# Optimization experiments

Measured on AMD Instinct MI355X. Metric: run time of the kernel, lower is better.

## Reference

```python
import jax, jax.numpy as jnp
import numpy as np

B, S, HID = 4, 1024, 2048
H, KV, D = 16, 4, 128  # query heads, kv heads, head_dim
ROPE_THETA = 1e6


def setup_inputs() -> dict:
    key = jax.random.key(0)
    ks = jax.random.split(key, 5)
    x = jax.random.normal(ks[0], (B, S, HID), dtype=jnp.float32)
    wq = jax.random.normal(ks[1], (HID, H * D), dtype=jnp.float32) / np.sqrt(HID)
    wk = jax.random.normal(ks[2], (HID, KV * D), dtype=jnp.float32) / np.sqrt(HID)
    wv = jax.random.normal(ks[3], (HID, KV * D), dtype=jnp.float32) / np.sqrt(HID)
    wo = jax.random.normal(ks[4], (H * D, HID), dtype=jnp.float32) / np.sqrt(H * D)
    # RoPE tables: freqs duplicated to head_dim (HF convention matching rotate_half)
    inv_freq = 1.0 / (ROPE_THETA ** (jnp.arange(0, D, 2, dtype=jnp.float32) / D))
    ang = jnp.arange(S, dtype=jnp.float32)[:, None] * inv_freq[None, :]  # [S, D/2]
    emb = jnp.concatenate([ang, ang], axis=-1)  # [S, D]
    return {"x": x, "cos": jnp.cos(emb), "sin": jnp.sin(emb),
            "wq": wq, "wk": wk, "wv": wv, "wo": wo}


def _rotate_half(t):
    half = t.shape[-1] // 2
    return jnp.concatenate([-t[..., half:], t[..., :half]], axis=-1)


def reference(x, cos, sin, wq, wk, wv, wo):
    b, s, _ = x.shape
    q = (x @ wq).reshape(b, s, H, D)
    k = (x @ wk).reshape(b, s, KV, D)
    v = (x @ wv).reshape(b, s, KV, D)
    # RoPE: cos/sin [S,D] broadcast over heads (unsqueeze_dim=1 -> [S,1,D])
    c = cos[:, None, :]
    sn = sin[:, None, :]
    q = q * c + _rotate_half(q) * sn
    k = k * c + _rotate_half(k) * sn
    # repeat_kv: each kv head repeated n_repeat times consecutively
    rep = H // KV
    k = jnp.repeat(k, rep, axis=2)  # [B,S,H,D]
    v = jnp.repeat(v, rep, axis=2)
    # [B,H,S,D]
    q = q.transpose(0, 2, 1, 3)
    k = k.transpose(0, 2, 1, 3)
    v = v.transpose(0, 2, 1, 3)
    scores = jnp.einsum("bhqd,bhkd->bhqk", q, k) / jnp.sqrt(jnp.float32(D))
    causal = jnp.tril(jnp.ones((s, s), dtype=bool))
    scores = jnp.where(causal, scores, -jnp.inf)
    probs = jax.nn.softmax(scores.astype(jnp.float32), axis=-1).astype(q.dtype)
    out = jnp.einsum("bhqk,bhkd->bhqd", probs, v)
    out = out.transpose(0, 2, 1, 3).reshape(b, s, H * D)
    return out @ wo
```

## Files before the change

kernel.cpp:

```cpp
#include <hip/hip_runtime.h>

typedef __attribute__((ext_vector_type(8))) __bf16 bf16x8;
typedef __attribute__((ext_vector_type(4))) __bf16 bf16x4;
typedef __attribute__((ext_vector_type(4))) float f32x4;

#define DEV static __device__ __forceinline__

DEV void gload_lds16(const void* g, void* l) {
  __builtin_amdgcn_global_load_lds((const __attribute__((address_space(1))) void*)g,
                                   (__attribute__((address_space(3))) void*)l, 16, 0, 0);
}

DEV void lgkm0_sb() {
  asm volatile("s_waitcnt lgkmcnt(0)" ::: "memory");
  __builtin_amdgcn_sched_barrier(0);
}

__global__ void cvt_kernel(const float* __restrict__ src, __bf16* __restrict__ dst, int n) {
  int i = (blockIdx.x * 256 + threadIdx.x) * 8;
  if (i >= n) return;
  float4 a = *(const float4*)(src + i);
  float4 b = *(const float4*)(src + i + 4);
  bf16x8 o;
  o[0] = (__bf16)a.x; o[1] = (__bf16)a.y; o[2] = (__bf16)a.z; o[3] = (__bf16)a.w;
  o[4] = (__bf16)b.x; o[5] = (__bf16)b.y; o[6] = (__bf16)b.z; o[7] = (__bf16)b.w;
  *(bf16x8*)(dst + i) = o;
}

__global__ void tcvt_kernel(const float* __restrict__ src, __bf16* __restrict__ dst, int K, int N) {
  __shared__ float tile[32][33];
  int k0 = blockIdx.y * 32, n0 = blockIdx.x * 32;
  int tx = threadIdx.x & 31, ty = threadIdx.x >> 5;
  #pragma unroll
  for (int i = 0; i < 32; i += 8)
    tile[ty + i][tx] = src[(size_t)(k0 + ty + i) * N + n0 + tx];
  __syncthreads();
  #pragma unroll
  for (int i = 0; i < 32; i += 8)
    dst[(size_t)(n0 + ty + i) * K + k0 + tx] = (__bf16)tile[tx][ty + i];
}

__global__ void vt_kernel(const __bf16* __restrict__ QKV, __bf16* __restrict__ VT) {
  __shared__ __bf16 t[32][33];
  int sx = blockIdx.x;
  int dx = blockIdx.y;
  int bk = blockIdx.z;
  int b = bk >> 2, kvh = bk & 3;
  int tx = threadIdx.x & 31, ty = threadIdx.x >> 5;
  #pragma unroll
  for (int i = 0; i < 32; i += 8)
    t[ty + i][tx] = QKV[(size_t)(b * 1024 + sx * 32 + ty + i) * 3072 + 2560 + kvh * 128 + dx * 32 + tx];
  __syncthreads();
  #pragma unroll
  for (int i = 0; i < 32; i += 8)
    VT[((size_t)bk * 128 + dx * 32 + ty + i) * 1024 + sx * 32 + tx] = t[tx][ty + i];
}

template <int BM, typename OutT>
__global__ __launch_bounds__(512, 2) void gemm8p(const __bf16* __restrict__ A,
                                                 const __bf16* __restrict__ Bt,
                                                 OutT* __restrict__ C,
                                                 int M, int N, int K) {
  constexpr int ABYTES = BM * 64 * 2;
  constexpr int BBYTES = 256 * 64 * 2;
  constexpr int MH = BM / 64;
  __shared__ alignas(1024) char smem[2 * (ABYTES + BBYTES)];

  const int tid = threadIdx.x;
  const int l = tid & 63, w = tid >> 6;
  const int wr = w >> 2, wc = w & 3;
  const int g = l >> 4, ln = l & 15;

  const int nbx = gridDim.x;
  const int nwg = nbx * gridDim.y;
  int lin = blockIdx.y * nbx + blockIdx.x;
  lin = (lin & 7) * (nwg >> 3) + (lin >> 3);
  const int brow = (lin / nbx) * BM, bcol = (lin % nbx) * 256;

  const __bf16* Ag = A + (size_t)brow * K;
  const __bf16* Bg = Bt + (size_t)bcol * K;
  const int NT = K / 64;

  auto Abuf = [&](int buf) -> char* { return smem + buf * ABYTES; };
  auto Bbuf = [&](int buf) -> char* { return smem + 2 * ABYTES + buf * BBYTES; };

  f32x4 acc[2 * MH][4] = {};

  auto chunk = [&](const __bf16* gb, char* lb, int ktc, int sub) {
    int r16 = l >> 2;
    int colb = ((l & 3) * 16) ^ (((l >> 5) & 1) << 5);
    int row = (sub >> 1) * 16 + r16;
    gload_lds16(gb + (size_t)row * K + ktc * 64 + (sub & 1) * 32 + (colb >> 1),
                lb + sub * 1024 + l * 16);
  };
  auto stA0 = [&](int ktc, int buf) {
    if constexpr (BM == 256) {
      #pragma unroll
      for (int i = 0; i < 2; ++i) { int idx = i * 8 + w; chunk(Ag, Abuf(buf), ktc, (idx >> 3) * 16 + (idx & 7)); }
    } else {
      chunk(Ag, Abuf(buf), ktc, (w >> 2) * 8 + (w & 3));
    }
  };
  auto stA1 = [&](int ktc, int buf) {
    if constexpr (BM == 256) {
      #pragma unroll
      for (int i = 0; i < 2; ++i) { int idx = i * 8 + w; chunk(Ag, Abuf(buf), ktc, 8 + (idx >> 3) * 16 + (idx & 7)); }
    } else {
      chunk(Ag, Abuf(buf), ktc, 4 + (w >> 2) * 8 + (w & 3));
    }
  };
  auto stB0 = [&](int ktc, int buf) {
    #pragma unroll
    for (int i = 0; i < 2; ++i) { int idx = i * 8 + w; chunk(Bg, Bbuf(buf), ktc, (idx >> 2) * 8 + (idx & 3)); }
  };
  auto stB1 = [&](int ktc, int buf) {
    #pragma unroll
    for (int i = 0; i < 2; ++i) { int idx = i * 8 + w; chunk(Bg, Bbuf(buf), ktc, 4 + (idx >> 2) * 8 + (idx & 3)); }
  };

  auto ldA = [&](int buf, int m, int kk) -> bf16x8 {
    int sub = (wr * (BM / 32) + m) * 2 + kk;
    return *(const bf16x8*)(Abuf(buf) + sub * 1024 + ln * 64 + ((g * 16) ^ (((ln >> 3) & 1) << 5)));
  };
  auto ldB = [&](int buf, int n, int kk) -> bf16x8 {
    int sub = (wc * 4 + n) * 2 + kk;
    return *(const bf16x8*)(Bbuf(buf) + sub * 1024 + ln * 64 + ((g * 16) ^ (((ln >> 3) & 1) << 5)));
  };

  auto vmw = [&](int which) {
    if constexpr (BM == 256) {
      if (which == 0) asm volatile("s_waitcnt vmcnt(10)" ::: "memory");
      else if (which == 1) asm volatile("s_waitcnt vmcnt(12)" ::: "memory");
      else asm volatile("s_waitcnt vmcnt(12)" ::: "memory");
    } else {
      if (which == 0) asm volatile("s_waitcnt vmcnt(7)" ::: "memory");
      else if (which == 1) asm volatile("s_waitcnt vmcnt(9)" ::: "memory");
      else asm volatile("s_waitcnt vmcnt(9)" ::: "memory");
    }
    __builtin_amdgcn_sched_barrier(0);
  };
  auto bar = [&]() {
    __builtin_amdgcn_sched_barrier(0);
    __builtin_amdgcn_s_barrier();
    __builtin_amdgcn_sched_barrier(0);
  };

  stA0(0, 0); stB0(0, 0); stB1(0, 0); stA1(0, 0);
  stA0(1, 1); stB0(1, 1); stB1(1, 1); stA1(1, 1);
  vmw(2);
  bar();

  bf16x8 af[MH][2], bf[4][2];

  for (int kt = 0; kt < NT; ++kt) {
    const int buf = kt & 1;
    const int ktc = (kt + 2) & 31;

    #pragma unroll
    for (int m = 0; m < MH; ++m) { af[m][0] = ldA(buf, m, 0); af[m][1] = ldA(buf, m, 1); }
    #pragma unroll
    for (int n = 0; n < 2; ++n) { bf[n][0] = ldB(buf, n, 0); bf[n][1] = ldB(buf, n, 1); }
    bar();
    lgkm0_sb();
    __builtin_amdgcn_s_setprio(1);
    #pragma unroll
    for (int m = 0; m < MH; ++m)
      #pragma unroll
      for (int n = 0; n < 2; ++n)
        #pragma unroll
        for (int kk = 0; kk < 2; ++kk)
          acc[m][n] = __builtin_amdgcn_mfma_f32_16x16x32_bf16(af[m][kk], bf[n][kk], acc[m][n], 0, 0, 0);
    __builtin_amdgcn_s_setprio(0);
    vmw(0);
    bar();

    #pragma unroll
    for (int n = 2; n < 4; ++n) { bf[n][0] = ldB(buf, n, 0); bf[n][1] = ldB(buf, n, 1); }
    stA0(ktc, buf); stB0(ktc, buf);
    bar();
    lgkm0_sb();
    __builtin_amdgcn_s_setprio(1);
    #pragma unroll
    for (int m = 0; m < MH; ++m)
      #pragma unroll
      for (int n = 2; n < 4; ++n)
        #pragma unroll
        for (int kk = 0; kk < 2; ++kk)
          acc[m][n] = __builtin_amdgcn_mfma_f32_16x16x32_bf16(af[m][kk], bf[n][kk], acc[m][n], 0, 0, 0);
    __builtin_amdgcn_s_setprio(0);
    vmw(1);
    bar();

    #pragma unroll
    for (int m = 0; m < MH; ++m) { af[m][0] = ldA(buf, MH + m, 0); af[m][1] = ldA(buf, MH + m, 1); }
    stB1(ktc, buf);
    bar();
    lgkm0_sb();
    __builtin_amdgcn_s_setprio(1);
    #pragma unroll
    for (int m = 0; m < MH; ++m)
      #pragma unroll
      for (int n = 0; n < 2; ++n)
        #pragma unroll
        for (int kk = 0; kk < 2; ++kk)
          acc[MH + m][n] = __builtin_amdgcn_mfma_f32_16x16x32_bf16(af[m][kk], bf[n][kk], acc[MH + m][n], 0, 0, 0);
    __builtin_amdgcn_s_setprio(0);
    bar();

    stA1(ktc, buf);
    bar();
    lgkm0_sb();
    __builtin_amdgcn_s_setprio(1);
    #pragma unroll
    for (int m = 0; m < MH; ++m)
      #pragma unroll
      for (int n = 2; n < 4; ++n)
        #pragma unroll
        for (int kk = 0; kk < 2; ++kk)
          acc[MH + m][n] = __builtin_amdgcn_mfma_f32_16x16x32_bf16(af[m][kk], bf[n][kk], acc[MH + m][n], 0, 0, 0);
    __builtin_amdgcn_s_setprio(0);
    vmw(2);
    bar();
  }

  #pragma unroll
  for (int mi = 0; mi < 2 * MH; ++mi)
    #pragma unroll
    for (int n = 0; n < 4; ++n)
      #pragma unroll
      for (int j = 0; j < 4; ++j) {
        size_t r = brow + wr * (BM / 2) + mi * 16 + g * 4 + j;
        size_t c = bcol + wc * 64 + n * 16 + ln;
        C[r * N + c] = (OutT)acc[mi][n][j];
      }
}

__global__ __launch_bounds__(512, 2) void gemm8p_qkv(const __bf16* __restrict__ A,
                                                     const __bf16* __restrict__ Bt,
                                                     __bf16* __restrict__ C,
                                                     int M, int N, int K) {
  constexpr int ABYTES = 256 * 64 * 2;
  constexpr int BBYTES = 192 * 64 * 2;
  __shared__ alignas(1024) char smem[2 * (ABYTES + BBYTES)];

  const int tid = threadIdx.x;
  const int l = tid & 63, w = tid >> 6;
  const int wr = w >> 2, wc = w & 3;
  const int g = l >> 4, ln = l & 15;

  const int nbx = gridDim.x;
  const int nwg = nbx * gridDim.y;
  int lin = blockIdx.y * nbx + blockIdx.x;
  lin = (lin & 7) * (nwg >> 3) + (lin >> 3);
  const int brow = (lin / nbx) * 256, bcol = (lin % nbx) * 192;

  const __bf16* Ag = A + (size_t)brow * K;
  const __bf16* Bg = Bt + (size_t)bcol * K;
  const int NT = K / 64;

  auto Abuf = [&](int buf) -> char* { return smem + buf * ABYTES; };
  auto Bbuf = [&](int buf) -> char* { return smem + 2 * ABYTES + buf * BBYTES; };

  f32x4 acc[8][3] = {};

  auto chunk = [&](const __bf16* gb, char* lb, int ktc, int sub) {
    int r16 = l >> 2;
    int colb = ((l & 3) * 16) ^ (((l >> 5) & 1) << 5);
    int row = (sub >> 1) * 16 + r16;
    gload_lds16(gb + (size_t)row * K + ktc * 64 + (sub & 1) * 32 + (colb >> 1),
                lb + sub * 1024 + l * 16);
  };
  auto stA0 = [&](int ktc, int buf) {
    #pragma unroll
    for (int i = 0; i < 2; ++i) { int idx = i * 8 + w; chunk(Ag, Abuf(buf), ktc, (idx >> 3) * 16 + (idx & 7)); }
  };
  auto stA1 = [&](int ktc, int buf) {
    #pragma unroll
    for (int i = 0; i < 2; ++i) { int idx = i * 8 + w; chunk(Ag, Abuf(buf), ktc, 8 + (idx >> 3) * 16 + (idx & 7)); }
  };
  auto stBg0 = [&](int ktc, int buf) {
    #pragma unroll
    for (int i = 0; i < 2; ++i) {
      int t = i * 8 + w;
      int sub = ((t >> 2) * 3 + ((t >> 1) & 1)) * 2 + (t & 1);
      chunk(Bg, Bbuf(buf), ktc, sub);
    }
  };
  auto stBg1 = [&](int ktc, int buf) {
    int sub = ((w >> 1) * 3 + 2) * 2 + (w & 1);
    chunk(Bg, Bbuf(buf), ktc, sub);
  };

  auto ldA = [&](int buf, int m, int kk) -> bf16x8 {
    int sub = (wr * 8 + m) * 2 + kk;
    return *(const bf16x8*)(Abuf(buf) + sub * 1024 + ln * 64 + ((g * 16) ^ (((ln >> 3) & 1) << 5)));
  };
  auto ldB = [&](int buf, int nf, int kk) -> bf16x8 {
    int sub = (wc * 3 + nf) * 2 + kk;
    return *(const bf16x8*)(Bbuf(buf) + sub * 1024 + ln * 64 + ((g * 16) ^ (((ln >> 3) & 1) << 5)));
  };

  auto bar = [&]() {
    __builtin_amdgcn_sched_barrier(0);
    __builtin_amdgcn_s_barrier();
    __builtin_amdgcn_sched_barrier(0);
  };

  stA0(0, 0); stBg0(0, 0); stBg1(0, 0); stA1(0, 0);
  stA0(1, 1); stBg0(1, 1); stBg1(1, 1); stA1(1, 1);
  asm volatile("s_waitcnt vmcnt(10)" ::: "memory");
  __builtin_amdgcn_sched_barrier(0);
  bar();

  bf16x8 af[4][2], bfv[3][2];

  for (int kt = 0; kt < NT; ++kt) {
    const int buf = kt & 1;
    const int ktc = (kt + 2) & 31;

    #pragma unroll
    for (int m = 0; m < 4; ++m) { af[m][0] = ldA(buf, m, 0); af[m][1] = ldA(buf, m, 1); }
    #pragma unroll
    for (int nf = 0; nf < 2; ++nf) { bfv[nf][0] = ldB(buf, nf, 0); bfv[nf][1] = ldB(buf, nf, 1); }
    bar();
    lgkm0_sb();
    __builtin_amdgcn_s_setprio(1);
    #pragma unroll
    for (int m = 0; m < 4; ++m)
      #pragma unroll
      for (int nf = 0; nf < 2; ++nf)
        #pragma unroll
        for (int kk = 0; kk < 2; ++kk)
          acc[m][nf] = __builtin_amdgcn_mfma_f32_16x16x32_bf16(af[m][kk], bfv[nf][kk], acc[m][nf], 0, 0, 0);
    __builtin_amdgcn_s_setprio(0);
    asm volatile("s_waitcnt vmcnt(9)" ::: "memory");
    __builtin_amdgcn_sched_barrier(0);
    bar();

    bfv[2][0] = ldB(buf, 2, 0); bfv[2][1] = ldB(buf, 2, 1);
    stA0(ktc, buf); stBg0(ktc, buf);
    bar();
    lgkm0_sb();
    __builtin_amdgcn_s_setprio(1);
    #pragma unroll
    for (int m = 0; m < 4; ++m)
      #pragma unroll
      for (int kk = 0; kk < 2; ++kk)
        acc[m][2] = __builtin_amdgcn_mfma_f32_16x16x32_bf16(af[m][kk], bfv[2][kk], acc[m][2], 0, 0, 0);
    __builtin_amdgcn_s_setprio(0);
    asm volatile("s_waitcnt vmcnt(11)" ::: "memory");
    __builtin_amdgcn_sched_barrier(0);
    bar();

    #pragma unroll
    for (int m = 0; m < 4; ++m) { af[m][0] = ldA(buf, 4 + m, 0); af[m][1] = ldA(buf, 4 + m, 1); }
    stBg1(ktc, buf);
    bar();
    lgkm0_sb();
    __builtin_amdgcn_s_setprio(1);
    #pragma unroll
    for (int m = 0; m < 4; ++m)
      #pragma unroll
      for (int nf = 0; nf < 2; ++nf)
        #pragma unroll
        for (int kk = 0; kk < 2; ++kk)
          acc[4 + m][nf] = __builtin_amdgcn_mfma_f32_16x16x32_bf16(af[m][kk], bfv[nf][kk], acc[4 + m][nf], 0, 0, 0);
    __builtin_amdgcn_s_setprio(0);
    bar();

    stA1(ktc, buf);
    bar();
    lgkm0_sb();
    __builtin_amdgcn_s_setprio(1);
    #pragma unroll
    for (int m = 0; m < 4; ++m)
      #pragma unroll
      for (int kk = 0; kk < 2; ++kk)
        acc[4 + m][2] = __builtin_amdgcn_mfma_f32_16x16x32_bf16(af[m][kk], bfv[2][kk], acc[4 + m][2], 0, 0, 0);
    __builtin_amdgcn_s_setprio(0);
    asm volatile("s_waitcnt vmcnt(10)" ::: "memory");
    __builtin_amdgcn_sched_barrier(0);
    bar();
  }

  #pragma unroll
  for (int mi = 0; mi < 8; ++mi)
    #pragma unroll
    for (int nf = 0; nf < 3; ++nf)
      #pragma unroll
      for (int j = 0; j < 4; ++j) {
        size_t r = brow + wr * 128 + mi * 16 + g * 4 + j;
        size_t c = bcol + wc * 48 + nf * 16 + ln;
        C[r * N + c] = (__bf16)acc[mi][nf][j];
      }
}

__global__ void rope_kernel(__bf16* __restrict__ QKV, const float* __restrict__ cosb,
                            const float* __restrict__ sinb) {
  int gid = blockIdx.x * 256 + threadIdx.x;
  int p = gid & 15;
  int ht = gid >> 4;
  int hc = ht % 20;
  int tok = ht / 20;
  int s = tok & 1023;
  int colb = hc < 16 ? hc * 128 : 2048 + (hc - 16) * 128;
  __bf16* base = QKV + (size_t)tok * 3072 + colb;
  int d0 = p * 4;
  const float* cr = cosb + s * 128;
  const float* sr = sinb + s * 128;
  float x0[4], x1[4];
  #pragma unroll
  for (int j = 0; j < 4; ++j) {
    x0[j] = (float)base[d0 + j];
    x1[j] = (float)base[d0 + 64 + j];
  }
  #pragma unroll
  for (int j = 0; j < 4; ++j) {
    float n0 = x0[j] * cr[d0 + j] - x1[j] * sr[d0 + j];
    float n1 = x1[j] * cr[d0 + 64 + j] + x0[j] * sr[d0 + 64 + j];
    base[d0 + j] = (__bf16)n0;
    base[d0 + 64 + j] = (__bf16)n1;
  }
}

__global__ __launch_bounds__(256, 2) void attn_kernel(const __bf16* __restrict__ QKV,
                                                      const __bf16* __restrict__ VT,
                                                      __bf16* __restrict__ AO) {
  __shared__ __bf16 Kl[2][64 * 128];
  __shared__ __bf16 Vt[128 * 64];
  __shared__ __bf16 Pl[4][16 * 72];

  const int tid = threadIdx.x, l = tid & 63, w = tid >> 6;
  const int h = blockIdx.y, b = blockIdx.z;
  const int kvh = h >> 2;
  const int g = l >> 4, ln = l & 15;
  const __bf16* VTg = VT + (size_t)(b * 4 + kvh) * 128 * 1024;
  const float scsc = 0.08838834764831845f;

  auto stageK = [&](int buf, int kt) {
    const __bf16* Kg = QKV + (size_t)(b * 1024 + kt * 64) * 3072 + 2048 + kvh * 128;
    #pragma unroll
    for (int i = 0; i < 4; ++i) {
      int r = i * 16 + (tid >> 4);
      int c = tid & 15;
      int csw = c ^ (r & 7);
      gload_lds16(Kg + (size_t)r * 3072 + csw * 8, (char*)&Kl[buf][0] + i * 4096 + tid * 16);
    }
  };
  auto stageV = [&](int kt) {
    #pragma unroll
    for (int i = 0; i < 4; ++i) {
      int ci = i * 256 + tid;
      int row = ci >> 3;
      int c = ci & 7;
      int csw = c ^ (row & 7);
      gload_lds16(VTg + (size_t)row * 1024 + kt * 64 + csw * 8, (char*)Vt + (size_t)ci * 16);
    }
  };

  #pragma unroll 1
  for (int pass = 0; pass < 2; ++pass) {
    const int qt = pass ? 15 - (int)blockIdx.x : (int)blockIdx.x;
    const size_t tokQ = (size_t)b * 1024 + qt * 64;

    bf16x8 qf[4];
    {
      const __bf16* qp = QKV + (tokQ + w * 16 + ln) * 3072 + h * 128;
      #pragma unroll
      for (int ks = 0; ks < 4; ++ks) qf[ks] = *(const bf16x8*)(qp + ks * 32 + g * 8);
    }

    float mrow = -1e30f, lrow = 0.f;
    f32x4 acco[8] = {};

    stageK(0, 0);
    int cur = 0;

    for (int kt = 0; kt <= qt; ++kt) {
      __syncthreads();

      stageV(kt);
      if (kt < qt) stageK(cur ^ 1, kt + 1);

      f32x4 accs[4] = {};
      __builtin_amdgcn_s_setprio(1);
      #pragma unroll
      for (int cb = 0; cb < 4; ++cb) {
        int row = cb * 16 + ln;
        #pragma unroll
        for (int ks = 0; ks < 4; ++ks) {
          bf16x8 kb = *(const bf16x8*)((const char*)&Kl[cur][0] + row * 256 +
                                       (((ks * 4 + g) ^ (row & 7)) * 16));
          accs[cb] = __builtin_amdgcn_mfma_f32_16x16x32_bf16(kb, qf[ks], accs[cb], 0, 0, 0);
        }
      }
      __builtin_amdgcn_s_setprio(0);

      const bool diag = (kt == qt);
      #pragma unroll
      for (int cb = 0; cb < 4; ++cb)
        #pragma unroll
        for (int j = 0; j < 4; ++j) {
          float s = accs[cb][j] * scsc;
          if (diag && (cb * 16 + g * 4 + j > w * 16 + ln)) s = -1e30f;
          accs[cb][j] = s;
        }

      float mt = accs[0][0];
      #pragma unroll
      for (int cb = 0; cb < 4; ++cb)
        #pragma unroll
        for (int j = 0; j < 4; ++j) mt = fmaxf(mt, accs[cb][j]);
      mt = fmaxf(mt, __shfl_xor(mt, 16, 64));
      mt = fmaxf(mt, __shfl_xor(mt, 32, 64));
      float mnew = fmaxf(mrow, mt);
      float corr = __expf(mrow - mnew);
      mrow = mnew;
      float rs = 0.f;
      #pragma unroll
      for (int cb = 0; cb < 4; ++cb)
        #pragma unroll
        for (int j = 0; j < 4; ++j) {
          float p = __expf(accs[cb][j] - mnew);
          accs[cb][j] = p;
          rs += p;
        }
      rs += __shfl_xor(rs, 16, 64);
      rs += __shfl_xor(rs, 32, 64);
      lrow = lrow * corr + rs;
      #pragma unroll
      for (int n = 0; n < 8; ++n)
        #pragma unroll
        for (int j = 0; j < 4; ++j) acco[n][j] *= corr;

      #pragma unroll
      for (int cb = 0; cb < 4; ++cb) {
        bf16x4 pw;
        #pragma unroll
        for (int j = 0; j < 4; ++j) pw[j] = (__bf16)accs[cb][j];
        *(bf16x4*)(&Pl[w][ln * 72 + cb * 16 + g * 4]) = pw;
      }

      __syncthreads();

      __builtin_amdgcn_s_setprio(1);
      #pragma unroll
      for (int sc = 0; sc < 2; ++sc) {
        bf16x8 pa = *(const bf16x8*)(&Pl[w][ln * 72 + sc * 32 + g * 8]);
        #pragma unroll
        for (int n = 0; n < 8; ++n) {
          int row = n * 16 + ln;
          bf16x8 vb = *(const bf16x8*)((const char*)Vt + row * 128 +
                                       (((sc * 4 + g) ^ (row & 7)) * 16));
          acco[n] = __builtin_amdgcn_mfma_f32_16x16x32_bf16(vb, pa, acco[n], 0, 0, 0);
        }
      }
      __builtin_amdgcn_s_setprio(0);
      cur ^= 1;
    }

    float rl = 1.f / lrow;
    size_t r = tokQ + w * 16 + ln;
    #pragma unroll
    for (int n = 0; n < 8; ++n) {
      bf16x4 ov;
      #pragma unroll
      for (int j = 0; j < 4; ++j) ov[j] = (__bf16)(acco[n][j] * rl);
      *(bf16x4*)(&AO[r * 2048 + h * 128 + n * 16 + g * 4]) = ov;
    }
  }
}

extern "C" void kernel_launch(void* const* d_in, const int* in_sizes, int n_in,
                              void* d_out, int out_size, void* d_ws, size_t ws_size,
                              hipStream_t stream) {
  const float* x    = (const float*)d_in[0];
  const float* cosb = (const float*)d_in[1];
  const float* sinb = (const float*)d_in[2];
  const float* wq   = (const float*)d_in[3];
  const float* wk   = (const float*)d_in[4];
  const float* wv   = (const float*)d_in[5];
  const float* wo   = (const float*)d_in[6];
  float* out = (float*)d_out;

  char* ws = (char*)d_ws;
  const size_t OFF_XB    = 0;
  const size_t OFF_WQKVT = OFF_XB + 16777216;
  const size_t OFF_WOT   = OFF_WQKVT + 12582912;
  const size_t OFF_QKV   = OFF_WOT + 8388608;
  const size_t OFF_AO    = OFF_QKV + 25165824;
  const size_t OFF_VT    = OFF_XB;

  __bf16* Xb    = (__bf16*)(ws + OFF_XB);
  __bf16* WqkvT = (__bf16*)(ws + OFF_WQKVT);
  __bf16* WoT   = (__bf16*)(ws + OFF_WOT);
  __bf16* QKVb  = (__bf16*)(ws + OFF_QKV);
  __bf16* AOb   = (__bf16*)(ws + OFF_AO);
  __bf16* VTb   = (__bf16*)(ws + OFF_VT);

  cvt_kernel<<<4096 * 2048 / 8 / 256, 256, 0, stream>>>(x, Xb, 4096 * 2048);
  tcvt_kernel<<<dim3(64, 64), 256, 0, stream>>>(wq, WqkvT, 2048, 2048);
  tcvt_kernel<<<dim3(16, 64), 256, 0, stream>>>(wk, WqkvT + (size_t)2048 * 2048, 2048, 512);
  tcvt_kernel<<<dim3(16, 64), 256, 0, stream>>>(wv, WqkvT + (size_t)2560 * 2048, 2048, 512);
  tcvt_kernel<<<dim3(64, 64), 256, 0, stream>>>(wo, WoT, 2048, 2048);
  gemm8p_qkv<<<dim3(16, 16), 512, 0, stream>>>(Xb, WqkvT, QKVb, 4096, 3072, 2048);
  vt_kernel<<<dim3(32, 4, 16), 256, 0, stream>>>(QKVb, VTb);
  rope_kernel<<<4096 * 20 * 16 / 256, 256, 0, stream>>>(QKVb, cosb, sinb);
  attn_kernel<<<dim3(8, 16, 4), 256, 0, stream>>>(QKVb, VTb, AOb);
  gemm8p<128, float><<<dim3(8, 32), 512, 0, stream>>>(AOb, WoT, out, 4096, 2048, 2048);
}
```

Before: 172.3 us.

## Fuse Q RoPE into attention and replace output GEMM with 256x128 tile kernel

The separate RoPE pass now handles only the 4 K heads; Q rotation moves into the attention kernel, applied in registers right after the Q fragments are loaded. This avoids a read-modify-write of the Q columns through global memory, at the cost of extra cos/sin loads inside attention. The output projection also switches from the 128x256-tile gemm8p to a new gemm2p kernel with 256x128 tiles, a two-phase k-loop and a different prefetch schedule, launched with 256 workgroups.

```diff
diff --git a/kernel.cpp b/kernel.cpp
--- a/kernel.cpp
+++ b/kernel.cpp
@@ -56,185 +56,6 @@
     VT[((size_t)bk * 128 + dx * 32 + ty + i) * 1024 + sx * 32 + tx] = t[tx][ty + i];
 }
 
-template <int BM, typename OutT>
-__global__ __launch_bounds__(512, 2) void gemm8p(const __bf16* __restrict__ A,
-                                                 const __bf16* __restrict__ Bt,
-                                                 OutT* __restrict__ C,
-                                                 int M, int N, int K) {
-  constexpr int ABYTES = BM * 64 * 2;
-  constexpr int BBYTES = 256 * 64 * 2;
-  constexpr int MH = BM / 64;
-  __shared__ alignas(1024) char smem[2 * (ABYTES + BBYTES)];
-
-  const int tid = threadIdx.x;
-  const int l = tid & 63, w = tid >> 6;
-  const int wr = w >> 2, wc = w & 3;
-  const int g = l >> 4, ln = l & 15;
-
-  const int nbx = gridDim.x;
-  const int nwg = nbx * gridDim.y;
-  int lin = blockIdx.y * nbx + blockIdx.x;
-  lin = (lin & 7) * (nwg >> 3) + (lin >> 3);
-  const int brow = (lin / nbx) * BM, bcol = (lin % nbx) * 256;
-
-  const __bf16* Ag = A + (size_t)brow * K;
-  const __bf16* Bg = Bt + (size_t)bcol * K;
-  const int NT = K / 64;
-
-  auto Abuf = [&](int buf) -> char* { return smem + buf * ABYTES; };
-  auto Bbuf = [&](int buf) -> char* { return smem + 2 * ABYTES + buf * BBYTES; };
-
-  f32x4 acc[2 * MH][4] = {};
-
-  auto chunk = [&](const __bf16* gb, char* lb, int ktc, int sub) {
-    int r16 = l >> 2;
-    int colb = ((l & 3) * 16) ^ (((l >> 5) & 1) << 5);
-    int row = (sub >> 1) * 16 + r16;
-    gload_lds16(gb + (size_t)row * K + ktc * 64 + (sub & 1) * 32 + (colb >> 1),
-                lb + sub * 1024 + l * 16);
-  };
-  auto stA0 = [&](int ktc, int buf) {
-    if constexpr (BM == 256) {
-      #pragma unroll
-      for (int i = 0; i < 2; ++i) { int idx = i * 8 + w; chunk(Ag, Abuf(buf), ktc, (idx >> 3) * 16 + (idx & 7)); }
-    } else {
-      chunk(Ag, Abuf(buf), ktc, (w >> 2) * 8 + (w & 3));
-    }
-  };
-  auto stA1 = [&](int ktc, int buf) {
-    if constexpr (BM == 256) {
-      #pragma unroll
-      for (int i = 0; i < 2; ++i) { int idx = i * 8 + w; chunk(Ag, Abuf(buf), ktc, 8 + (idx >> 3) * 16 + (idx & 7)); }
-    } else {
-      chunk(Ag, Abuf(buf), ktc, 4 + (w >> 2) * 8 + (w & 3));
-    }
-  };
-  auto stB0 = [&](int ktc, int buf) {
-    #pragma unroll
-    for (int i = 0; i < 2; ++i) { int idx = i * 8 + w; chunk(Bg, Bbuf(buf), ktc, (idx >> 2) * 8 + (idx & 3)); }
-  };
-  auto stB1 = [&](int ktc, int buf) {
-    #pragma unroll
-    for (int i = 0; i < 2; ++i) { int idx = i * 8 + w; chunk(Bg, Bbuf(buf), ktc, 4 + (idx >> 2) * 8 + (idx & 3)); }
-  };
-
-  auto ldA = [&](int buf, int m, int kk) -> bf16x8 {
-    int sub = (wr * (BM / 32) + m) * 2 + kk;
-    return *(const bf16x8*)(Abuf(buf) + sub * 1024 + ln * 64 + ((g * 16) ^ (((ln >> 3) & 1) << 5)));
-  };
-  auto ldB = [&](int buf, int n, int kk) -> bf16x8 {
-    int sub = (wc * 4 + n) * 2 + kk;
-    return *(const bf16x8*)(Bbuf(buf) + sub * 1024 + ln * 64 + ((g * 16) ^ (((ln >> 3) & 1) << 5)));
-  };
-
-  auto vmw = [&](int which) {
-    if constexpr (BM == 256) {
-      if (which == 0) asm volatile("s_waitcnt vmcnt(10)" ::: "memory");
-      else if (which == 1) asm volatile("s_waitcnt vmcnt(12)" ::: "memory");
-      else asm volatile("s_waitcnt vmcnt(12)" ::: "memory");
-    } else {
-      if (which == 0) asm volatile("s_waitcnt vmcnt(7)" ::: "memory");
-      else if (which == 1) asm volatile("s_waitcnt vmcnt(9)" ::: "memory");
-      else asm volatile("s_waitcnt vmcnt(9)" ::: "memory");
-    }
-    __builtin_amdgcn_sched_barrier(0);
-  };
-  auto bar = [&]() {
-    __builtin_amdgcn_sched_barrier(0);
-    __builtin_amdgcn_s_barrier();
-    __builtin_amdgcn_sched_barrier(0);
-  };
-
-  stA0(0, 0); stB0(0, 0); stB1(0, 0); stA1(0, 0);
-  stA0(1, 1); stB0(1, 1); stB1(1, 1); stA1(1, 1);
-  vmw(2);
-  bar();
-
-  bf16x8 af[MH][2], bf[4][2];
-
-  for (int kt = 0; kt < NT; ++kt) {
-    const int buf = kt & 1;
-    const int ktc = (kt + 2) & 31;
-
-    #pragma unroll
-    for (int m = 0; m < MH; ++m) { af[m][0] = ldA(buf, m, 0); af[m][1] = ldA(buf, m, 1); }
-    #pragma unroll
-    for (int n = 0; n < 2; ++n) { bf[n][0] = ldB(buf, n, 0); bf[n][1] = ldB(buf, n, 1); }
-    bar();
-    lgkm0_sb();
-    __builtin_amdgcn_s_setprio(1);
-    #pragma unroll
-    for (int m = 0; m < MH; ++m)
-      #pragma unroll
-      for (int n = 0; n < 2; ++n)
-        #pragma unroll
-        for (int kk = 0; kk < 2; ++kk)
-          acc[m][n] = __builtin_amdgcn_mfma_f32_16x16x32_bf16(af[m][kk], bf[n][kk], acc[m][n], 0, 0, 0);
-    __builtin_amdgcn_s_setprio(0);
-    vmw(0);
-    bar();
-
-    #pragma unroll
-    for (int n = 2; n < 4; ++n) { bf[n][0] = ldB(buf, n, 0); bf[n][1] = ldB(buf, n, 1); }
-    stA0(ktc, buf); stB0(ktc, buf);
-    bar();
-    lgkm0_sb();
-    __builtin_amdgcn_s_setprio(1);
-    #pragma unroll
-    for (int m = 0; m < MH; ++m)
-      #pragma unroll
-      for (int n = 2; n < 4; ++n)
-        #pragma unroll
-        for (int kk = 0; kk < 2; ++kk)
-          acc[m][n] = __builtin_amdgcn_mfma_f32_16x16x32_bf16(af[m][kk], bf[n][kk], acc[m][n], 0, 0, 0);
-    __builtin_amdgcn_s_setprio(0);
-    vmw(1);
-    bar();
-
-    #pragma unroll
-    for (int m = 0; m < MH; ++m) { af[m][0] = ldA(buf, MH + m, 0); af[m][1] = ldA(buf, MH + m, 1); }
-    stB1(ktc, buf);
-    bar();
-    lgkm0_sb();
-    __builtin_amdgcn_s_setprio(1);
-    #pragma unroll
-    for (int m = 0; m < MH; ++m)
-      #pragma unroll
-      for (int n = 0; n < 2; ++n)
-        #pragma unroll
-        for (int kk = 0; kk < 2; ++kk)
-          acc[MH + m][n] = __builtin_amdgcn_mfma_f32_16x16x32_bf16(af[m][kk], bf[n][kk], acc[MH + m][n], 0, 0, 0);
-    __builtin_amdgcn_s_setprio(0);
-    bar();
-
-    stA1(ktc, buf);
-    bar();
-    lgkm0_sb();
-    __builtin_amdgcn_s_setprio(1);
-    #pragma unroll
-    for (int m = 0; m < MH; ++m)
-      #pragma unroll
-      for (int n = 2; n < 4; ++n)
-        #pragma unroll
-        for (int kk = 0; kk < 2; ++kk)
-          acc[MH + m][n] = __builtin_amdgcn_mfma_f32_16x16x32_bf16(af[m][kk], bf[n][kk], acc[MH + m][n], 0, 0, 0);
-    __builtin_amdgcn_s_setprio(0);
-    vmw(2);
-    bar();
-  }
-
-  #pragma unroll
-  for (int mi = 0; mi < 2 * MH; ++mi)
-    #pragma unroll
-    for (int n = 0; n < 4; ++n)
-      #pragma unroll
-      for (int j = 0; j < 4; ++j) {
-        size_t r = brow + wr * (BM / 2) + mi * 16 + g * 4 + j;
-        size_t c = bcol + wc * 64 + n * 16 + ln;
-        C[r * N + c] = (OutT)acc[mi][n][j];
-      }
-}
-
 __global__ __launch_bounds__(512, 2) void gemm8p_qkv(const __bf16* __restrict__ A,
                                                      const __bf16* __restrict__ Bt,
                                                      __bf16* __restrict__ C,
@@ -395,16 +216,144 @@
       }
 }
 
-__global__ void rope_kernel(__bf16* __restrict__ QKV, const float* __restrict__ cosb,
-                            const float* __restrict__ sinb) {
+__global__ __launch_bounds__(512, 2) void gemm2p(const __bf16* __restrict__ A,
+                                                 const __bf16* __restrict__ Bt,
+                                                 float* __restrict__ C,
+                                                 int M, int N, int K) {
+  constexpr int ABYTES = 256 * 64 * 2;
+  constexpr int BBYTES = 128 * 64 * 2;
+  __shared__ alignas(1024) char smem[2 * (ABYTES + BBYTES)];
+
+  const int tid = threadIdx.x;
+  const int l = tid & 63, w = tid >> 6;
+  const int wr = w >> 1, wc = w & 1;
+  const int g = l >> 4, ln = l & 15;
+
+  const int nbx = gridDim.x;
+  const int nwg = nbx * gridDim.y;
+  int lin = blockIdx.y * nbx + blockIdx.x;
+  lin = (lin & 7) * (nwg >> 3) + (lin >> 3);
+  const int brow = (lin / nbx) * 256, bcol = (lin % nbx) * 128;
+
+  const __bf16* Ag = A + (size_t)brow * K;
+  const __bf16* Bg = Bt + (size_t)bcol * K;
+  const int NT = K / 64;
+
+  auto Abuf = [&](int buf) -> char* { return smem + buf * ABYTES; };
+  auto Bbuf = [&](int buf) -> char* { return smem + 2 * ABYTES + buf * BBYTES; };
+
+  f32x4 acc[4][4] = {};
+
+  auto chunk = [&](const __bf16* gb, char* lb, int ktc, int sub) {
+    int r16 = l >> 2;
+    int colb = ((l & 3) * 16) ^ (((l >> 5) & 1) << 5);
+    int row = (sub >> 1) * 16 + r16;
+    gload_lds16(gb + (size_t)row * K + ktc * 64 + (sub & 1) * 32 + (colb >> 1),
+                lb + sub * 1024 + l * 16);
+  };
+  auto stAp0 = [&](int ktc, int buf) {
+    #pragma unroll
+    for (int i = 0; i < 2; ++i) { int t = i * 8 + w; chunk(Ag, Abuf(buf), ktc, (t >> 2) * 8 + (t & 3)); }
+  };
+  auto stAp1 = [&](int ktc, int buf) {
+    #pragma unroll
+    for (int i = 0; i < 2; ++i) { int t = i * 8 + w; chunk(Ag, Abuf(buf), ktc, (t >> 2) * 8 + 4 + (t & 3)); }
+  };
+  auto stB = [&](int ktc, int buf) {
+    #pragma unroll
+    for (int i = 0; i < 2; ++i) { int t = i * 8 + w; chunk(Bg, Bbuf(buf), ktc, t); }
+  };
+
+  auto ldA = [&](int buf, int mi, int kk) -> bf16x8 {
+    int sub = (wr * 4 + mi) * 2 + kk;
+    return *(const bf16x8*)(Abuf(buf) + sub * 1024 + ln * 64 + ((g * 16) ^ (((ln >> 3) & 1) << 5)));
+  };
+  auto ldB = [&](int buf, int nf, int kk) -> bf16x8 {
+    int sub = (wc * 4 + nf) * 2 + kk;
+    return *(const bf16x8*)(Bbuf(buf) + sub * 1024 + ln * 64 + ((g * 16) ^ (((ln >> 3) & 1) << 5)));
+  };
+
+  auto vm6 = [&]() {
+    asm volatile("s_waitcnt vmcnt(6)" ::: "memory");
+    __builtin_amdgcn_sched_barrier(0);
+  };
+  auto bar = [&]() {
+    __builtin_amdgcn_sched_barrier(0);
+    __builtin_amdgcn_s_barrier();
+    __builtin_amdgcn_sched_barrier(0);
+  };
+
+  stAp0(0, 0); stB(0, 0);
+  stAp1(0, 0);
+  stAp0(1, 1); stB(1, 1);
+  vm6();
+  bar();
+
+  bf16x8 af[2][2], bfv[4][2];
+
+  for (int kt = 0; kt < NT; ++kt) {
+    const int buf = kt & 1;
+    const int ktc1 = (kt + 1) & 31;
+    const int ktc2 = (kt + 2) & 31;
+
+    #pragma unroll
+    for (int mi = 0; mi < 2; ++mi) { af[mi][0] = ldA(buf, mi, 0); af[mi][1] = ldA(buf, mi, 1); }
+    #pragma unroll
+    for (int nf = 0; nf < 4; ++nf) { bfv[nf][0] = ldB(buf, nf, 0); bfv[nf][1] = ldB(buf, nf, 1); }
+    stAp1(ktc1, buf ^ 1);
+    bar();
+    lgkm0_sb();
+    __builtin_amdgcn_s_setprio(1);
+    #pragma unroll
+    for (int mi = 0; mi < 2; ++mi)
+      #pragma unroll
+      for (int nf = 0; nf < 4; ++nf)
+        #pragma unroll
+        for (int kk = 0; kk < 2; ++kk)
+          acc[mi][nf] = __builtin_amdgcn_mfma_f32_16x16x32_bf16(af[mi][kk], bfv[nf][kk], acc[mi][nf], 0, 0, 0);
+    __builtin_amdgcn_s_setprio(0);
+    vm6();
+    bar();
+
+    #pragma unroll
+    for (int mi = 0; mi < 2; ++mi) { af[mi][0] = ldA(buf, 2 + mi, 0); af[mi][1] = ldA(buf, 2 + mi, 1); }
+    stAp0(ktc2, buf); stB(ktc2, buf);
+    bar();
+    lgkm0_sb();
+    __builtin_amdgcn_s_setprio(1);
+    #pragma unroll
+    for (int mi = 0; mi < 2; ++mi)
+      #pragma unroll
+      for (int nf = 0; nf < 4; ++nf)
+        #pragma unroll
+        for (int kk = 0; kk < 2; ++kk)
+          acc[2 + mi][nf] = __builtin_amdgcn_mfma_f32_16x16x32_bf16(af[mi][kk], bfv[nf][kk], acc[2 + mi][nf], 0, 0, 0);
+    __builtin_amdgcn_s_setprio(0);
+    vm6();
+    bar();
+  }
+
+  #pragma unroll
+  for (int mi = 0; mi < 4; ++mi)
+    #pragma unroll
+    for (int nf = 0; nf < 4; ++nf)
+      #pragma unroll
+      for (int j = 0; j < 4; ++j) {
+        size_t r = brow + wr * 64 + mi * 16 + g * 4 + j;
+        size_t c = bcol + wc * 64 + nf * 16 + ln;
+        C[r * N + c] = acc[mi][nf][j];
+      }
+}
+
+__global__ void ropek_kernel(__bf16* __restrict__ QKV, const float* __restrict__ cosb,
+                             const float* __restrict__ sinb) {
   int gid = blockIdx.x * 256 + threadIdx.x;
   int p = gid & 15;
   int ht = gid >> 4;
-  int hc = ht % 20;
-  int tok = ht / 20;
+  int hc = ht & 3;
+  int tok = ht >> 2;
   int s = tok & 1023;
-  int colb = hc < 16 ? hc * 128 : 2048 + (hc - 16) * 128;
-  __bf16* base = QKV + (size_t)tok * 3072 + colb;
+  __bf16* base = QKV + (size_t)tok * 3072 + 2048 + hc * 128;
   int d0 = p * 4;
   const float* cr = cosb + s * 128;
   const float* sr = sinb + s * 128;
@@ -425,6 +374,8 @@
 
 __global__ __launch_bounds__(256, 2) void attn_kernel(const __bf16* __restrict__ QKV,
                                                       const __bf16* __restrict__ VT,
+                                                      const float* __restrict__ cosb,
+                                                      const float* __restrict__ sinb,
                                                       __bf16* __restrict__ AO) {
   __shared__ __bf16 Kl[2][64 * 128];
   __shared__ __bf16 Vt[128 * 64];
@@ -462,12 +413,26 @@
   for (int pass = 0; pass < 2; ++pass) {
     const int qt = pass ? 15 - (int)blockIdx.x : (int)blockIdx.x;
     const size_t tokQ = (size_t)b * 1024 + qt * 64;
+    const int srow = qt * 64 + w * 16 + ln;
 
     bf16x8 qf[4];
     {
       const __bf16* qp = QKV + (tokQ + w * 16 + ln) * 3072 + h * 128;
-      #pragma unroll
-      for (int ks = 0; ks < 4; ++ks) qf[ks] = *(const bf16x8*)(qp + ks * 32 + g * 8);
+      bf16x8 qraw[4];
+      #pragma unroll
+      for (int ks = 0; ks < 4; ++ks) qraw[ks] = *(const bf16x8*)(qp + ks * 32 + g * 8);
+      const float* cr = cosb + (size_t)srow * 128;
+      const float* sr = sinb + (size_t)srow * 128;
+      #pragma unroll
+      for (int ks2 = 0; ks2 < 2; ++ks2)
+        #pragma unroll
+        for (int j = 0; j < 8; ++j) {
+          int d = ks2 * 32 + g * 8 + j;
+          float lo = (float)qraw[ks2][j], hi = (float)qraw[ks2 + 2][j];
+          float c0 = cr[d], s0 = sr[d];
+          qf[ks2][j]     = (__bf16)(lo * c0 - hi * s0);
+          qf[ks2 + 2][j] = (__bf16)(hi * c0 + lo * s0);
+        }
     }
 
     float mrow = -1e30f, lrow = 0.f;
@@ -605,7 +570,7 @@
   tcvt_kernel<<<dim3(64, 64), 256, 0, stream>>>(wo, WoT, 2048, 2048);
   gemm8p_qkv<<<dim3(16, 16), 512, 0, stream>>>(Xb, WqkvT, QKVb, 4096, 3072, 2048);
   vt_kernel<<<dim3(32, 4, 16), 256, 0, stream>>>(QKVb, VTb);
-  rope_kernel<<<4096 * 20 * 16 / 256, 256, 0, stream>>>(QKVb, cosb, sinb);
-  attn_kernel<<<dim3(8, 16, 4), 256, 0, stream>>>(QKVb, VTb, AOb);
-  gemm8p<128, float><<<dim3(8, 32), 512, 0, stream>>>(AOb, WoT, out, 4096, 2048, 2048);
-}
+  ropek_kernel<<<4096 * 4 * 16 / 256, 256, 0, stream>>>(QKVb, cosb, sinb);
+  attn_kernel<<<dim3(8, 16, 4), 256, 0, stream>>>(QKVb, VTb, cosb, sinb, AOb);
+  gemm2p<<<dim3(16, 16), 512, 0, stream>>>(AOb, WoT, out, 4096, 2048, 2048);
+}
```

Measured after the change: 171.5 us. No clear change (-0.5%).
